# Optimization experiments

Measured on AMD Instinct MI355X. Metric: run time of the kernel, lower is better.

The kernel has to match this reference:

```python
import jax, jax.numpy as jnp
import numpy as np

B = 4        # number of point clouds (equal-size contiguous batches)
P = 8192     # points per cloud
C_IN = 64
C_OUT = 64
K = 16       # kNN neighbors (includes the point itself, as in PyG knn)
EPS = 1e-5
NEG_SLOPE = 0.2


def setup_inputs() -> dict:
    key = jax.random.key(0)
    k1, k2, k3 = jax.random.split(key, 3)
    x = jax.random.normal(k1, (B * P, C_IN), dtype=jnp.float32)
    batch = jnp.repeat(jnp.arange(B, dtype=jnp.int64), P)  # sorted, equal sizes
    W = jax.random.normal(k2, (2 * C_IN, C_OUT), dtype=jnp.float32) * (1.0 / np.sqrt(2 * C_IN))
    b = jax.random.normal(k3, (C_OUT,), dtype=jnp.float32) * 0.01
    gamma = jnp.ones((C_OUT,), dtype=jnp.float32)
    beta = jnp.zeros((C_OUT,), dtype=jnp.float32)
    return {"x": x, "batch": batch, "W": W, "b": b, "gamma": gamma, "beta": beta}


def _edgeconv(x, W, b, gamma, beta):
    xb = x.reshape(B, P, C_IN)
    # per-cloud pairwise squared distances: [B, P, P]
    sq = jnp.sum(xb * xb, axis=-1)
    d = sq[:, :, None] + sq[:, None, :] - 2.0 * jnp.einsum("bpc,bqc->bpq", xb, xb)
    # k nearest neighbors (smallest distance, self included)
    _, idx = jax.lax.top_k(-d, K)                      # [B, P, K]
    xj = jax.vmap(lambda pts, ind: pts[ind])(xb, idx)  # [B, P, K, C_IN]
    xi = xb[:, :, None, :]
    e = jnp.concatenate([jnp.broadcast_to(xi, xj.shape), xj - xi], axis=-1)  # [B,P,K,2C]
    # edge MLP: Linear -> BatchNorm1d (training-mode batch stats over all edges) -> LeakyReLU
    h = jnp.einsum("bpke,eo->bpko", e, W) + b          # [B, P, K, C_OUT]
    hf = h.reshape(-1, C_OUT)
    mean = jnp.mean(hf, axis=0)
    var = jnp.mean(hf * hf, axis=0) - mean * mean      # biased variance (torch BN)
    hn = (h - mean) * jax.lax.rsqrt(var + EPS) * gamma + beta
    a = jnp.where(hn >= 0, hn, NEG_SLOPE * hn)
    # max aggregation over neighbors
    return jnp.max(a, axis=2).reshape(B * P, C_OUT)


def reference(x, batch, W, b, gamma, beta):
    # `batch` encodes B equal-size contiguous clouds; kNN is computed per cloud.
    return _edgeconv(x, W, b, gamma, beta)
```

## Files before the change

### kernel.cpp

```cpp
#include <hip/hip_runtime.h>
#include <cfloat>

#define BATCH 4
#define P 8192
#define C 64
#define KNN 16
#define NPTS (BATCH * P)
#define NEDGE (NPTS * KNN)
#define EPSV 1e-5f
#define SLOPE 0.2f
#define NQ 2
#define QCOLS (P / NQ)

typedef __attribute__((ext_vector_type(8))) short bf16x8;
typedef __attribute__((ext_vector_type(16))) float f32x16;


__device__ __forceinline__ unsigned short f2bf(float f) {
    unsigned u = __float_as_uint(f);
    u += 0x7FFFu + ((u >> 16) & 1u);
    return (unsigned short)(u >> 16);
}
__device__ __forceinline__ float bf2f(unsigned short s) {
    return __uint_as_float(((unsigned)s) << 16);
}

__global__ void prep_frag(const float* __restrict__ x, uint4* __restrict__ xfh,
                          uint4* __restrict__ xfm, uint4* __restrict__ xfl,
                          float* __restrict__ sq) {
    __shared__ float part[32][9];
    int tid = threadIdx.x;
    int ptl = tid >> 3, j8 = tid & 7;
    int g = blockIdx.x;
    int p = g * 32 + ptl;
    const float4* xp = (const float4*)(x + (size_t)p * C + j8 * 8);
    float4 a = xp[0], b = xp[1];
    float v[8] = {a.x, a.y, a.z, a.w, b.x, b.y, b.z, b.w};
    unsigned short hs[8], ms[8], ls[8];
    float ssum = 0.f;
#pragma unroll
    for (int e = 0; e < 8; ++e) {
        float xv = v[e];
        ssum = fmaf(xv, xv, ssum);
        unsigned short h = f2bf(xv);
        float r1 = xv - bf2f(h);
        unsigned short m = f2bf(r1);
        float r2 = r1 - bf2f(m);
        unsigned short l = f2bf(r2);
        hs[e] = h; ms[e] = m; ls[e] = l;
    }
    int dst = (g * 4 + (j8 >> 1)) * 64 + ptl + 32 * (j8 & 1);
    uint4 ph, pm, pl;
    ph.x = (unsigned)hs[0] | ((unsigned)hs[1] << 16);
    ph.y = (unsigned)hs[2] | ((unsigned)hs[3] << 16);
    ph.z = (unsigned)hs[4] | ((unsigned)hs[5] << 16);
    ph.w = (unsigned)hs[6] | ((unsigned)hs[7] << 16);
    pm.x = (unsigned)ms[0] | ((unsigned)ms[1] << 16);
    pm.y = (unsigned)ms[2] | ((unsigned)ms[3] << 16);
    pm.z = (unsigned)ms[4] | ((unsigned)ms[5] << 16);
    pm.w = (unsigned)ms[6] | ((unsigned)ms[7] << 16);
    pl.x = (unsigned)ls[0] | ((unsigned)ls[1] << 16);
    pl.y = (unsigned)ls[2] | ((unsigned)ls[3] << 16);
    pl.z = (unsigned)ls[4] | ((unsigned)ls[5] << 16);
    pl.w = (unsigned)ls[6] | ((unsigned)ls[7] << 16);
    xfh[dst] = ph; xfm[dst] = pm; xfl[dst] = pl;
    part[ptl][j8] = ssum;
    __syncthreads();
    if (j8 == 0) {
        float s = 0.f;
#pragma unroll
        for (int k = 0; k < 8; ++k) s += part[ptl][k];
        sq[p] = s;
    }
}

__global__ __launch_bounds__(256, 4) void knn_kernel(const uint4* __restrict__ xfh,
                                                     const uint4* __restrict__ xfm,
                                                     const uint4* __restrict__ xfl,
                                                     const float* __restrict__ sq,
                                                     float* __restrict__ pv,
                                                     int* __restrict__ pi) {
    __shared__ float bufv[64 * 65];
    __shared__ int   bufi[64 * 65];
    __shared__ int   idL[64 * 17];
    __shared__ int   cntL[64];
    __shared__ float worstL[64];

    int tid = threadIdx.x;
    int b = blockIdx.x & 3;
    int t = blockIdx.x >> 2;
    int tile = t & 127;
    int half = t >> 7;
    int bglob = b * P;
    int r0 = tile * 64;
    int colbase = half * QCOLS;
    int w = tid >> 6, lane = tid & 63;
    int wr = w & 1, wc = w >> 1;

    if (tid < 64) { cntL[tid] = 0; worstL[tid] = FLT_MAX; }

    int gA = ((bglob + r0) >> 5) + wr;
    bf16x8 Ah[4], Am[4], Al[4];
#pragma unroll
    for (int kk = 0; kk < 4; ++kk) {
        Ah[kk] = __builtin_bit_cast(bf16x8, xfh[(gA * 4 + kk) * 64 + lane]);
        Am[kk] = __builtin_bit_cast(bf16x8, xfm[(gA * 4 + kk) * 64 + lane]);
        Al[kk] = __builtin_bit_cast(bf16x8, xfl[(gA * 4 + kk) * 64 + lane]);
    }

    float tv[16];
    float worst = FLT_MAX;
#pragma unroll
    for (int j = 0; j < 16; ++j) tv[j] = FLT_MAX;
    int rown = w * 16 + (lane & 15);
    bool owner = (lane < 16);

    int rbase = wr * 32 + 4 * (lane >> 5);
    int colq = wc * 32 + (lane & 31);
    __syncthreads();

    for (int chunk = 0; chunk < QCOLS / 64; ++chunk) {
        int c0 = colbase + chunk * 64;
        int gB = ((bglob + c0) >> 5) + wc;
        bf16x8 Bh[4], Bm[4], Bl[4];
#pragma unroll
        for (int kk = 0; kk < 4; ++kk) {
            Bh[kk] = __builtin_bit_cast(bf16x8, xfh[(gB * 4 + kk) * 64 + lane]);
            Bm[kk] = __builtin_bit_cast(bf16x8, xfm[(gB * 4 + kk) * 64 + lane]);
            Bl[kk] = __builtin_bit_cast(bf16x8, xfl[(gB * 4 + kk) * 64 + lane]);
        }
        float sc = sq[bglob + c0 + colq];

        f32x16 acc0, acc1;
#pragma unroll
        for (int i = 0; i < 16; ++i) { acc0[i] = 0.f; acc1[i] = 0.f; }
#pragma unroll
        for (int kk = 0; kk < 4; ++kk) {
            acc0 = __builtin_amdgcn_mfma_f32_32x32x16_bf16(Ah[kk], Bh[kk], acc0, 0, 0, 0);
            acc1 = __builtin_amdgcn_mfma_f32_32x32x16_bf16(Ah[kk], Bm[kk], acc1, 0, 0, 0);
            acc0 = __builtin_amdgcn_mfma_f32_32x32x16_bf16(Am[kk], Bh[kk], acc0, 0, 0, 0);
            acc1 = __builtin_amdgcn_mfma_f32_32x32x16_bf16(Am[kk], Bm[kk], acc1, 0, 0, 0);
            acc0 = __builtin_amdgcn_mfma_f32_32x32x16_bf16(Ah[kk], Bl[kk], acc0, 0, 0, 0);
            acc1 = __builtin_amdgcn_mfma_f32_32x32x16_bf16(Al[kk], Bh[kk], acc1, 0, 0, 0);
        }

        if (chunk == 0) {
#pragma unroll
            for (int reg = 0; reg < 16; ++reg) {
                float s = fmaf(-2.f, acc0[reg] + acc1[reg], sc);
                int row = rbase + (reg & 3) + 8 * (reg >> 2);
                bufv[row * 65 + colq] = s;
            }
        } else {
            float4 twA[4];
#pragma unroll
            for (int g4 = 0; g4 < 4; ++g4)
                twA[g4] = *(const float4*)&worstL[rbase + 8 * g4];
            int colg = bglob + c0 + colq;
#pragma unroll
            for (int reg = 0; reg < 16; ++reg) {
                float s = fmaf(-2.f, acc0[reg] + acc1[reg], sc);
                float tW = ((const float*)&twA[reg >> 2])[reg & 3];
                if (s < tW) {
                    int row = rbase + (reg & 3) + 8 * (reg >> 2);
                    int slot = atomicAdd(&cntL[row], 1);
                    bufv[row * 65 + slot] = s;
                    bufi[row * 65 + slot] = colg;
                }
            }
        }
        __syncthreads();

        if (owner) {
            int n = (chunk == 0) ? 64 : cntL[rown];
            for (int k = 0; k < n; ++k) {
                float s = bufv[rown * 65 + k];
                if (s < worst) {
                    float mx = tv[0];
                    int pos = 0;
#pragma unroll
                    for (int j = 1; j < 16; ++j) {
                        bool g = tv[j] > mx;
                        mx = g ? tv[j] : mx;
                        pos = g ? j : pos;
                    }
#pragma unroll
                    for (int j = 0; j < 16; ++j)
                        if (j == pos) tv[j] = s;
                    idL[rown * 17 + pos] = (chunk == 0) ? (bglob + colbase + k)
                                                        : bufi[rown * 65 + k];
                    float nw = fmaxf(fmaxf(fmaxf(tv[0], tv[1]), fmaxf(tv[2], tv[3])),
                                     fmaxf(fmaxf(tv[4], tv[5]), fmaxf(tv[6], tv[7])));
                    nw = fmaxf(nw, fmaxf(fmaxf(fmaxf(tv[8], tv[9]), fmaxf(tv[10], tv[11])),
                                         fmaxf(fmaxf(tv[12], tv[13]), fmaxf(tv[14], tv[15]))));
                    worst = nw;
                }
            }
            cntL[rown] = 0;
            worstL[rown] = worst;
        }
        __syncthreads();
    }

    if (owner) {
        size_t o = (((size_t)(bglob + r0 + rown)) * NQ + half) * KNN;
#pragma unroll
        for (int j = 0; j < 16; ++j) {
            pv[o + j] = tv[j];
            pi[o + j] = idL[rown * 17 + j];
        }
    }
}

__global__ void merge_kernel(const float* __restrict__ pv, const int* __restrict__ pi,
                             int* __restrict__ idx_out) {
    __shared__ float mv[128 * 33];
    __shared__ int   mi[128 * 33];
    int tid = threadIdx.x;
    int lr = tid & 127, q = tid >> 7;
    int row = blockIdx.x * 128 + lr;
    size_t o = ((size_t)row * NQ + q) * KNN;
#pragma unroll
    for (int j = 0; j < 16; ++j) {
        mv[lr * 33 + q * 16 + j] = pv[o + j];
        mi[lr * 33 + q * 16 + j] = pi[o + j];
    }
    __syncthreads();
    if (tid < 128) {
        float tv[16];
        int ti[16];
        float worst = FLT_MAX;
#pragma unroll
        for (int j = 0; j < 16; ++j) { tv[j] = FLT_MAX; ti[j] = 0; }
        for (int e = 0; e < 32; ++e) {
            float s = mv[tid * 33 + e];
            if (s < worst) {
                float mx = tv[0];
                int pos = 0;
#pragma unroll
                for (int j = 1; j < 16; ++j) {
                    bool g = tv[j] > mx;
                    mx = g ? tv[j] : mx;
                    pos = g ? j : pos;
                }
#pragma unroll
                for (int j = 0; j < 16; ++j)
                    if (j == pos) { tv[j] = s; ti[j] = mi[tid * 33 + e]; }
                float nw = tv[0];
#pragma unroll
                for (int j = 1; j < 16; ++j) nw = fmaxf(nw, tv[j]);
                worst = nw;
            }
        }
        size_t oo = (size_t)row * KNN;
#pragma unroll
        for (int j = 0; j < 16; ++j) idx_out[oo + j] = ti[j];
    }
}

__global__ void prep_UV(const float* __restrict__ x, const float* __restrict__ W,
                        float* __restrict__ U, float* __restrict__ V) {
    __shared__ float Ws[128][64];
    __shared__ float xs[4][64];
    int tid = threadIdx.x;
    for (int i = tid; i < 128 * 64; i += 256) ((float*)Ws)[i] = W[i];
    int p0 = blockIdx.x * 4;
    int r = tid >> 6, c = tid & 63;
    xs[r][c] = x[(size_t)(p0 + r) * C + c];
    __syncthreads();
    float u = 0.f, v = 0.f;
#pragma unroll
    for (int k = 0; k < 64; ++k) {
        float xv = xs[r][k];
        float w1 = Ws[k][c];
        float w2 = Ws[64 + k][c];
        u = fmaf(xv, w1 - w2, u);
        v = fmaf(xv, w2, v);
    }
    size_t o = (size_t)(p0 + r) * C + c;
    U[o] = u;
    V[o] = v;
}

__global__ void stats_kernel(const float* __restrict__ U, const float* __restrict__ V,
                             const float* __restrict__ bias, const int* __restrict__ idx,
                             float* __restrict__ stats) {
    int tid = threadIdx.x;
    int c = tid & 63, kk = tid >> 6;
    int p0 = blockIdx.x * 32;
    float bc = bias[c];
    float sum = 0.f, sumsq = 0.f;
    for (int pp = 0; pp < 32; ++pp) {
        int p = p0 + pp;
        float u = U[(size_t)p * C + c] + bc;
#pragma unroll
        for (int k4 = 0; k4 < 4; ++k4) {
            int j = idx[(size_t)p * KNN + kk * 4 + k4];
            float h = u + V[(size_t)j * C + c];
            sum += h;
            sumsq = fmaf(h, h, sumsq);
        }
    }
    __shared__ float red[2][4][64];
    red[0][kk][c] = sum;
    red[1][kk][c] = sumsq;
    __syncthreads();
    if (tid < 64) {
        float s = red[0][0][tid] + red[0][1][tid] + red[0][2][tid] + red[0][3][tid];
        atomicAdd(&stats[tid], s);
    } else if (tid < 128) {
        int cc = tid - 64;
        float s = red[1][0][cc] + red[1][1][cc] + red[1][2][cc] + red[1][3][cc];
        atomicAdd(&stats[64 + cc], s);
    }
}

__global__ void finalize_kernel(const float* __restrict__ stats,
                                const float* __restrict__ gamma,
                                const float* __restrict__ beta,
                                float* __restrict__ sshift) {
    int c = threadIdx.x;
    const float N = (float)NEDGE;
    float mean = stats[c] / N;
    float var = stats[64 + c] / N - mean * mean;
    float s = gamma[c] * rsqrtf(var + EPSV);
    sshift[c] = s;
    sshift[64 + c] = beta[c] - mean * s;
}

__global__ void out_kernel(const float* __restrict__ U, const float* __restrict__ V,
                           const float* __restrict__ bias, const int* __restrict__ idx,
                           const float* __restrict__ sshift, float* __restrict__ out) {
    int tid = threadIdx.x;
    int c = tid & 63, g = tid >> 6;
    int p0 = blockIdx.x * 16;
    float s = sshift[c], t = sshift[64 + c];
    float bc = bias[c];
    for (int pp = g; pp < 16; pp += 4) {
        int p = p0 + pp;
        float mx = -FLT_MAX, mn = FLT_MAX;
#pragma unroll
        for (int k = 0; k < KNN; ++k) {
            int j = idx[(size_t)p * KNN + k];
            float v = V[(size_t)j * C + c];
            mx = fmaxf(mx, v);
            mn = fminf(mn, v);
        }
        float hsel = (s >= 0.f) ? mx : mn;
        float hn = fmaf(s, U[(size_t)p * C + c] + bc + hsel, t);
        out[(size_t)p * C + c] = (hn >= 0.f) ? hn : SLOPE * hn;
    }
}

extern "C" void kernel_launch(void* const* d_in, const int* in_sizes, int n_in,
                              void* d_out, int out_size, void* d_ws, size_t ws_size,
                              hipStream_t stream) {
    const float* x     = (const float*)d_in[0];
    const float* W     = (const float*)d_in[2];
    const float* bias  = (const float*)d_in[3];
    const float* gamma = (const float*)d_in[4];
    const float* beta  = (const float*)d_in[5];
    float* out = (float*)d_out;

    float* wsf    = (float*)d_ws;
    float* U      = wsf;
    float* V      = wsf + 2097152;
    uint4* xfh    = (uint4*)wsf;
    uint4* xfm    = (uint4*)(wsf + 1048576);
    uint4* xfl    = (uint4*)(wsf + 2097152);
    float* sq     = wsf + 4194304;
    float* stats  = wsf + 4227072;
    float* sshift = wsf + 4227200;
    int*   idx    = (int*)(wsf + 4227328);
    float* pv     = wsf + 4751616;
    int*   pi     = (int*)(wsf + 5800192);

    hipLaunchKernelGGL(prep_frag, dim3(NPTS / 32), dim3(256), 0, stream, x, xfh, xfm, xfl, sq);
    hipLaunchKernelGGL(knn_kernel, dim3(BATCH * (P / 64) * NQ), dim3(256), 0, stream,
                       (const uint4*)xfh, (const uint4*)xfm, (const uint4*)xfl, sq, pv, pi);
    hipLaunchKernelGGL(merge_kernel, dim3(NPTS / 128), dim3(256), 0, stream, pv, pi, idx);
    hipLaunchKernelGGL(prep_UV, dim3(NPTS / 4), dim3(256), 0, stream, x, W, U, V);
    hipMemsetAsync(stats, 0, 128 * sizeof(float), stream);
    hipLaunchKernelGGL(stats_kernel, dim3(NPTS / 32), dim3(256), 0, stream, U, V, bias, idx, stats);
    hipLaunchKernelGGL(finalize_kernel, dim3(1), dim3(64), 0, stream, stats, gamma, beta, sshift);
    hipLaunchKernelGGL(out_kernel, dim3(NPTS / 16), dim3(256), 0, stream, U, V, bias, idx, sshift, out);
}
```

Baseline: 571.3 us.

## Give each wave private kNN candidate buffers and drop block barriers

Each wave now keeps its own 32-row by 32-column top-k state in shared memory. That removes both __syncthreads per chunk and lets 32 lanes per wave do the insertion instead of 16. The partial result count per row doubles to four, so the merge kernel now merges 64 candidates per row, and the workspace for the partial indices is moved. B fragment loads are split into two halves separated by a scheduling barrier to cut register pressure. Candidate indices are stored as 16-bit column offsets. Correctness depends on intra-wave ordering of shared-memory writes and reads without an explicit barrier.

```diff
diff --git a/kernel.cpp b/kernel.cpp
--- a/kernel.cpp
+++ b/kernel.cpp
@@ -11,6 +11,7 @@
 #define SLOPE 0.2f
 #define NQ 2
 #define QCOLS (P / NQ)
+#define NPART 4
 
 typedef __attribute__((ext_vector_type(8))) short bf16x8;
 typedef __attribute__((ext_vector_type(16))) float f32x16;
@@ -80,11 +81,11 @@
                                                      const float* __restrict__ sq,
                                                      float* __restrict__ pv,
                                                      int* __restrict__ pi) {
-    __shared__ float bufv[64 * 65];
-    __shared__ int   bufi[64 * 65];
-    __shared__ int   idL[64 * 17];
-    __shared__ int   cntL[64];
-    __shared__ float worstL[64];
+    __shared__ float          bufv[4 * 32 * 33];
+    __shared__ unsigned short bufi[4 * 32 * 33];
+    __shared__ int            idL [4 * 32 * 17];
+    __shared__ int            cntL[4 * 32];
+    __shared__ float          worstL[4 * 32];
 
     int tid = threadIdx.x;
     int b = blockIdx.x & 3;
@@ -97,7 +98,13 @@
     int w = tid >> 6, lane = tid & 63;
     int wr = w & 1, wc = w >> 1;
 
-    if (tid < 64) { cntL[tid] = 0; worstL[tid] = FLT_MAX; }
+    float*          bufvW = bufv + w * (32 * 33);
+    unsigned short* bufiW = bufi + w * (32 * 33);
+    int*            idLW  = idL  + w * (32 * 17);
+    int*            cntW  = cntL + w * 32;
+    float*          worstW = worstL + w * 32;
+
+    if (lane < 32) { cntW[lane] = 0; worstW[lane] = FLT_MAX; }
 
     int gA = ((bglob + r0) >> 5) + wr;
     bf16x8 Ah[4], Am[4], Al[4];
@@ -112,69 +119,93 @@
     float worst = FLT_MAX;
 #pragma unroll
     for (int j = 0; j < 16; ++j) tv[j] = FLT_MAX;
-    int rown = w * 16 + (lane & 15);
-    bool owner = (lane < 16);
-
-    int rbase = wr * 32 + 4 * (lane >> 5);
-    int colq = wc * 32 + (lane & 31);
-    __syncthreads();
+
+    int rlbase = 4 * (lane >> 5);
+    int sub = lane & 31;
+    int colq = wc * 32 + sub;
 
     for (int chunk = 0; chunk < QCOLS / 64; ++chunk) {
         int c0 = colbase + chunk * 64;
         int gB = ((bglob + c0) >> 5) + wc;
-        bf16x8 Bh[4], Bm[4], Bl[4];
-#pragma unroll
-        for (int kk = 0; kk < 4; ++kk) {
-            Bh[kk] = __builtin_bit_cast(bf16x8, xfh[(gB * 4 + kk) * 64 + lane]);
-            Bm[kk] = __builtin_bit_cast(bf16x8, xfm[(gB * 4 + kk) * 64 + lane]);
-            Bl[kk] = __builtin_bit_cast(bf16x8, xfl[(gB * 4 + kk) * 64 + lane]);
-        }
         float sc = sq[bglob + c0 + colq];
 
         f32x16 acc0, acc1;
 #pragma unroll
         for (int i = 0; i < 16; ++i) { acc0[i] = 0.f; acc1[i] = 0.f; }
-#pragma unroll
-        for (int kk = 0; kk < 4; ++kk) {
-            acc0 = __builtin_amdgcn_mfma_f32_32x32x16_bf16(Ah[kk], Bh[kk], acc0, 0, 0, 0);
-            acc1 = __builtin_amdgcn_mfma_f32_32x32x16_bf16(Ah[kk], Bm[kk], acc1, 0, 0, 0);
-            acc0 = __builtin_amdgcn_mfma_f32_32x32x16_bf16(Am[kk], Bh[kk], acc0, 0, 0, 0);
-            acc1 = __builtin_amdgcn_mfma_f32_32x32x16_bf16(Am[kk], Bm[kk], acc1, 0, 0, 0);
-            acc0 = __builtin_amdgcn_mfma_f32_32x32x16_bf16(Ah[kk], Bl[kk], acc0, 0, 0, 0);
-            acc1 = __builtin_amdgcn_mfma_f32_32x32x16_bf16(Al[kk], Bh[kk], acc1, 0, 0, 0);
+
+        {
+            bf16x8 Bh0 = __builtin_bit_cast(bf16x8, xfh[(gB * 4 + 0) * 64 + lane]);
+            bf16x8 Bm0 = __builtin_bit_cast(bf16x8, xfm[(gB * 4 + 0) * 64 + lane]);
+            bf16x8 Bl0 = __builtin_bit_cast(bf16x8, xfl[(gB * 4 + 0) * 64 + lane]);
+            bf16x8 Bh1 = __builtin_bit_cast(bf16x8, xfh[(gB * 4 + 1) * 64 + lane]);
+            bf16x8 Bm1 = __builtin_bit_cast(bf16x8, xfm[(gB * 4 + 1) * 64 + lane]);
+            bf16x8 Bl1 = __builtin_bit_cast(bf16x8, xfl[(gB * 4 + 1) * 64 + lane]);
+            acc0 = __builtin_amdgcn_mfma_f32_32x32x16_bf16(Ah[0], Bh0, acc0, 0, 0, 0);
+            acc1 = __builtin_amdgcn_mfma_f32_32x32x16_bf16(Ah[0], Bm0, acc1, 0, 0, 0);
+            acc0 = __builtin_amdgcn_mfma_f32_32x32x16_bf16(Am[0], Bh0, acc0, 0, 0, 0);
+            acc1 = __builtin_amdgcn_mfma_f32_32x32x16_bf16(Am[0], Bm0, acc1, 0, 0, 0);
+            acc0 = __builtin_amdgcn_mfma_f32_32x32x16_bf16(Ah[0], Bl0, acc0, 0, 0, 0);
+            acc1 = __builtin_amdgcn_mfma_f32_32x32x16_bf16(Al[0], Bh0, acc1, 0, 0, 0);
+            acc0 = __builtin_amdgcn_mfma_f32_32x32x16_bf16(Ah[1], Bh1, acc0, 0, 0, 0);
+            acc1 = __builtin_amdgcn_mfma_f32_32x32x16_bf16(Ah[1], Bm1, acc1, 0, 0, 0);
+            acc0 = __builtin_amdgcn_mfma_f32_32x32x16_bf16(Am[1], Bh1, acc0, 0, 0, 0);
+            acc1 = __builtin_amdgcn_mfma_f32_32x32x16_bf16(Am[1], Bm1, acc1, 0, 0, 0);
+            acc0 = __builtin_amdgcn_mfma_f32_32x32x16_bf16(Ah[1], Bl1, acc0, 0, 0, 0);
+            acc1 = __builtin_amdgcn_mfma_f32_32x32x16_bf16(Al[1], Bh1, acc1, 0, 0, 0);
+        }
+        __builtin_amdgcn_sched_barrier(0);
+        {
+            bf16x8 Bh2 = __builtin_bit_cast(bf16x8, xfh[(gB * 4 + 2) * 64 + lane]);
+            bf16x8 Bm2 = __builtin_bit_cast(bf16x8, xfm[(gB * 4 + 2) * 64 + lane]);
+            bf16x8 Bl2 = __builtin_bit_cast(bf16x8, xfl[(gB * 4 + 2) * 64 + lane]);
+            bf16x8 Bh3 = __builtin_bit_cast(bf16x8, xfh[(gB * 4 + 3) * 64 + lane]);
+            bf16x8 Bm3 = __builtin_bit_cast(bf16x8, xfm[(gB * 4 + 3) * 64 + lane]);
+            bf16x8 Bl3 = __builtin_bit_cast(bf16x8, xfl[(gB * 4 + 3) * 64 + lane]);
+            acc0 = __builtin_amdgcn_mfma_f32_32x32x16_bf16(Ah[2], Bh2, acc0, 0, 0, 0);
+            acc1 = __builtin_amdgcn_mfma_f32_32x32x16_bf16(Ah[2], Bm2, acc1, 0, 0, 0);
+            acc0 = __builtin_amdgcn_mfma_f32_32x32x16_bf16(Am[2], Bh2, acc0, 0, 0, 0);
+            acc1 = __builtin_amdgcn_mfma_f32_32x32x16_bf16(Am[2], Bm2, acc1, 0, 0, 0);
+            acc0 = __builtin_amdgcn_mfma_f32_32x32x16_bf16(Ah[2], Bl2, acc0, 0, 0, 0);
+            acc1 = __builtin_amdgcn_mfma_f32_32x32x16_bf16(Al[2], Bh2, acc1, 0, 0, 0);
+            acc0 = __builtin_amdgcn_mfma_f32_32x32x16_bf16(Ah[3], Bh3, acc0, 0, 0, 0);
+            acc1 = __builtin_amdgcn_mfma_f32_32x32x16_bf16(Ah[3], Bm3, acc1, 0, 0, 0);
+            acc0 = __builtin_amdgcn_mfma_f32_32x32x16_bf16(Am[3], Bh3, acc0, 0, 0, 0);
+            acc1 = __builtin_amdgcn_mfma_f32_32x32x16_bf16(Am[3], Bm3, acc1, 0, 0, 0);
+            acc0 = __builtin_amdgcn_mfma_f32_32x32x16_bf16(Ah[3], Bl3, acc0, 0, 0, 0);
+            acc1 = __builtin_amdgcn_mfma_f32_32x32x16_bf16(Al[3], Bh3, acc1, 0, 0, 0);
         }
 
         if (chunk == 0) {
 #pragma unroll
             for (int reg = 0; reg < 16; ++reg) {
                 float s = fmaf(-2.f, acc0[reg] + acc1[reg], sc);
-                int row = rbase + (reg & 3) + 8 * (reg >> 2);
-                bufv[row * 65 + colq] = s;
+                int rl = rlbase + (reg & 3) + 8 * (reg >> 2);
+                bufvW[rl * 33 + sub] = s;
             }
         } else {
             float4 twA[4];
 #pragma unroll
             for (int g4 = 0; g4 < 4; ++g4)
-                twA[g4] = *(const float4*)&worstL[rbase + 8 * g4];
-            int colg = bglob + c0 + colq;
+                twA[g4] = *(const float4*)&worstW[rlbase + 8 * g4];
 #pragma unroll
             for (int reg = 0; reg < 16; ++reg) {
                 float s = fmaf(-2.f, acc0[reg] + acc1[reg], sc);
                 float tW = ((const float*)&twA[reg >> 2])[reg & 3];
                 if (s < tW) {
-                    int row = rbase + (reg & 3) + 8 * (reg >> 2);
-                    int slot = atomicAdd(&cntL[row], 1);
-                    bufv[row * 65 + slot] = s;
-                    bufi[row * 65 + slot] = colg;
+                    int rl = rlbase + (reg & 3) + 8 * (reg >> 2);
+                    int slot = atomicAdd(&cntW[rl], 1);
+                    bufvW[rl * 33 + slot] = s;
+                    bufiW[rl * 33 + slot] = (unsigned short)sub;
                 }
             }
         }
-        __syncthreads();
-
-        if (owner) {
-            int n = (chunk == 0) ? 64 : cntL[rown];
+
+        if (lane < 32) {
+            int n = (chunk == 0) ? 32 : cntW[lane];
+            int base = lane * 33;
+            int id0 = bglob + c0 + wc * 32;
             for (int k = 0; k < n; ++k) {
-                float s = bufv[rown * 65 + k];
+                float s = bufvW[base + k];
                 if (s < worst) {
                     float mx = tv[0];
                     int pos = 0;
@@ -187,8 +218,8 @@
 #pragma unroll
                     for (int j = 0; j < 16; ++j)
                         if (j == pos) tv[j] = s;
-                    idL[rown * 17 + pos] = (chunk == 0) ? (bglob + colbase + k)
-                                                        : bufi[rown * 65 + k];
+                    idLW[lane * 17 + pos] = (chunk == 0) ? (id0 + k)
+                                                         : (id0 + (int)bufiW[base + k]);
                     float nw = fmaxf(fmaxf(fmaxf(tv[0], tv[1]), fmaxf(tv[2], tv[3])),
                                      fmaxf(fmaxf(tv[4], tv[5]), fmaxf(tv[6], tv[7])));
                     nw = fmaxf(nw, fmaxf(fmaxf(fmaxf(tv[8], tv[9]), fmaxf(tv[10], tv[11])),
@@ -196,44 +227,44 @@
                     worst = nw;
                 }
             }
-            cntL[rown] = 0;
-            worstL[rown] = worst;
-        }
-        __syncthreads();
-    }
-
-    if (owner) {
-        size_t o = (((size_t)(bglob + r0 + rown)) * NQ + half) * KNN;
+            if (n > 0) { cntW[lane] = 0; worstW[lane] = worst; }
+        }
+        __builtin_amdgcn_sched_barrier(0);
+    }
+
+    if (lane < 32) {
+        int qq = half * 2 + wc;
+        size_t o = (((size_t)(bglob + r0 + wr * 32 + lane)) * NPART + qq) * KNN;
 #pragma unroll
         for (int j = 0; j < 16; ++j) {
             pv[o + j] = tv[j];
-            pi[o + j] = idL[rown * 17 + j];
+            pi[o + j] = idLW[lane * 17 + j];
         }
     }
 }
 
 __global__ void merge_kernel(const float* __restrict__ pv, const int* __restrict__ pi,
                              int* __restrict__ idx_out) {
-    __shared__ float mv[128 * 33];
-    __shared__ int   mi[128 * 33];
-    int tid = threadIdx.x;
-    int lr = tid & 127, q = tid >> 7;
-    int row = blockIdx.x * 128 + lr;
-    size_t o = ((size_t)row * NQ + q) * KNN;
+    __shared__ float mv[64][65];
+    __shared__ int   mi[64][65];
+    int tid = threadIdx.x;
+    int lr = tid & 63, q = tid >> 6;
+    int row = blockIdx.x * 64 + lr;
+    size_t o = ((size_t)row * NPART + q) * KNN;
 #pragma unroll
     for (int j = 0; j < 16; ++j) {
-        mv[lr * 33 + q * 16 + j] = pv[o + j];
-        mi[lr * 33 + q * 16 + j] = pi[o + j];
+        mv[lr][q * 16 + j] = pv[o + j];
+        mi[lr][q * 16 + j] = pi[o + j];
     }
     __syncthreads();
-    if (tid < 128) {
+    if (tid < 64) {
         float tv[16];
         int ti[16];
         float worst = FLT_MAX;
 #pragma unroll
         for (int j = 0; j < 16; ++j) { tv[j] = FLT_MAX; ti[j] = 0; }
-        for (int e = 0; e < 32; ++e) {
-            float s = mv[tid * 33 + e];
+        for (int e = 0; e < 64; ++e) {
+            float s = mv[tid][e];
             if (s < worst) {
                 float mx = tv[0];
                 int pos = 0;
@@ -245,7 +276,7 @@
                 }
 #pragma unroll
                 for (int j = 0; j < 16; ++j)
-                    if (j == pos) { tv[j] = s; ti[j] = mi[tid * 33 + e]; }
+                    if (j == pos) { tv[j] = s; ti[j] = mi[tid][e]; }
                 float nw = tv[0];
 #pragma unroll
                 for (int j = 1; j < 16; ++j) nw = fmaxf(nw, tv[j]);
@@ -373,12 +404,12 @@
     float* sshift = wsf + 4227200;
     int*   idx    = (int*)(wsf + 4227328);
     float* pv     = wsf + 4751616;
-    int*   pi     = (int*)(wsf + 5800192);
+    int*   pi     = (int*)(wsf + 6848768);
 
     hipLaunchKernelGGL(prep_frag, dim3(NPTS / 32), dim3(256), 0, stream, x, xfh, xfm, xfl, sq);
     hipLaunchKernelGGL(knn_kernel, dim3(BATCH * (P / 64) * NQ), dim3(256), 0, stream,
                        (const uint4*)xfh, (const uint4*)xfm, (const uint4*)xfl, sq, pv, pi);
-    hipLaunchKernelGGL(merge_kernel, dim3(NPTS / 128), dim3(256), 0, stream, pv, pi, idx);
+    hipLaunchKernelGGL(merge_kernel, dim3(NPTS / 64), dim3(256), 0, stream, pv, pi, idx);
     hipLaunchKernelGGL(prep_UV, dim3(NPTS / 4), dim3(256), 0, stream, x, W, U, V);
     hipMemsetAsync(stats, 0, 128 * sizeof(float), stream);
     hipLaunchKernelGGL(stats_kernel, dim3(NPTS / 32), dim3(256), 0, stream, U, V, bias, idx, stats);
```

After: 587.0 us. 2.7% more time.
